# Optimization experiments

Hardware: AMD Instinct MI355X
Metric: run time of the kernel (lower is better)

Reference implementation:

```python
import jax, jax.numpy as jnp
import numpy as np

EMB_DIM = 1024
NUM_HEADS = 16
HEAD_DIM = EMB_DIM // NUM_HEADS  # 64
B, S = 2, 2048


def setup_inputs() -> dict:
    key = jax.random.key(0)
    ks = jax.random.split(key, 9)
    scale = 1.0 / np.sqrt(EMB_DIM)
    return {
        "query": jax.random.normal(ks[0], (B, S, EMB_DIM), dtype=jnp.float32),
        "Wq": jax.random.normal(ks[1], (EMB_DIM, EMB_DIM), dtype=jnp.float32) * scale,
        "bq": jax.random.normal(ks[2], (EMB_DIM,), dtype=jnp.float32) * 0.01,
        "Wk": jax.random.normal(ks[3], (EMB_DIM, EMB_DIM), dtype=jnp.float32) * scale,
        "bk": jax.random.normal(ks[4], (EMB_DIM,), dtype=jnp.float32) * 0.01,
        "Wv": jax.random.normal(ks[5], (EMB_DIM, EMB_DIM), dtype=jnp.float32) * scale,
        "bv": jax.random.normal(ks[6], (EMB_DIM,), dtype=jnp.float32) * 0.01,
        "Wo": jax.random.normal(ks[7], (EMB_DIM, EMB_DIM), dtype=jnp.float32) * scale,
        "bo": jax.random.normal(ks[8], (EMB_DIM,), dtype=jnp.float32) * 0.01,
    }


def reference(query, Wq, bq, Wk, bk, Wv, bv, Wo, bo):
    # Self-attention path (key_value=None, mask=None in the original forward).
    b, s, _ = query.shape
    # torch nn.Linear: y = x @ W.T + b
    def proj(x, W, bias):
        y = jnp.einsum('bse,fe->bsf', x, W) + bias
        # [B,S,E] -> [B,H,S,D]
        return y.reshape(b, s, NUM_HEADS, HEAD_DIM).transpose(0, 2, 1, 3)

    q = proj(query, Wq, bq)
    k = proj(query, Wk, bk)
    v = proj(query, Wv, bv)

    scores = jnp.einsum('bhqd,bhkd->bhqk', q, k) / np.sqrt(HEAD_DIM).astype(np.float32)
    attn = jax.nn.softmax(scores, axis=-1)  # [B,H,S,S]
    out = jnp.einsum('bhqk,bhkd->bhqd', attn, v)
    out = out.transpose(0, 2, 1, 3).reshape(b, s, EMB_DIM)
    return jnp.einsum('bse,fe->bsf', out, Wo) + bo
```

## Files before the change

kernel.cpp:

```cpp
#include <hip/hip_runtime.h>
#include <hip/hip_bf16.h>

using bf16x4 = __attribute__((ext_vector_type(4))) short;
using short8 = __attribute__((ext_vector_type(8))) short;
using f32x4  = __attribute__((ext_vector_type(4))) float;
using u32x2  = __attribute__((ext_vector_type(2))) unsigned;

__device__ __forceinline__ short f2bf(float f) {
  unsigned u = __builtin_bit_cast(unsigned, f);
  u = (u + 0x7fffu + ((u >> 16) & 1u)) >> 16;
  return (short)u;
}
__device__ __forceinline__ unsigned pk2(float a, float b) {
  __hip_bfloat162 h = __float22bfloat162_rn(make_float2(a, b));
  unsigned u; __builtin_memcpy(&u, &h, 4);
  return u;
}
__device__ __forceinline__ void gload16(const short* g, short* l) {
  __builtin_amdgcn_global_load_lds(
      (const __attribute__((address_space(1))) unsigned int*)g,
      (__attribute__((address_space(3))) unsigned int*)l, 16, 0, 0);
}

constexpr int E  = 1024;
constexpr int SL = 2048;
constexpr int NB = 2;
constexpr int NH = 16;
constexpr int M  = NB * SL;

__global__ __launch_bounds__(256) void convert_kernel(
    const float* __restrict__ X,  const float* __restrict__ Wq,
    const float* __restrict__ Wk, const float* __restrict__ Wv,
    const float* __restrict__ Wo, short* __restrict__ out)
{
  const size_t i8 = ((size_t)blockIdx.x * 256 + threadIdx.x) * 8;
  const float* src;
  if (i8 < (size_t)(4u << 20)) {
    src = X + i8;
  } else {
    size_t r = i8 - (size_t)(4u << 20);
    int wi = (int)(r >> 20);
    size_t off = r & ((1u << 20) - 1);
    src = (wi == 0 ? Wq : wi == 1 ? Wk : wi == 2 ? Wv : Wo) + off;
  }
  f32x4 a = *(const f32x4*)src;
  f32x4 b = *(const f32x4*)(src + 4);
  short hb[8];
#pragma unroll
  for (int e = 0; e < 4; ++e) { hb[e] = f2bf(a[e]); hb[4 + e] = f2bf(b[e]); }
  *(short8*)(out + i8) = *(short8*)hb;
}

template <int TM, int TN, bool OUTF32, bool FUSEV>
__global__ __launch_bounds__(256) void gemm_kernel(
    const short* __restrict__ A0, const short* __restrict__ A1, const short* __restrict__ A2,
    const short* __restrict__ W0, const short* __restrict__ W1, const short* __restrict__ W2,
    const float* __restrict__ b0, const float* __restrict__ b1, const float* __restrict__ b2,
    void* __restrict__ Y0, void* __restrict__ Y1, void* __restrict__ Y2,
    float s0, float s1, float s2, int ld0, int ld1, int ld2)
{
  constexpr int BK = 32;
  constexpr int RA = TM / 64;
  constexpr int RB = TN / 64;
  constexpr int WM = TM / 2, WN = TN / 2;
  constexpr int NI = WM / 16, NJ = WN / 16;
  __shared__ alignas(16) short As[2][TM * BK];
  __shared__ alignas(16) short Bs[2][TN * BK];
  const int t = threadIdx.x;
  const int l = t & 63;
  const int w = t >> 6;
  const int c = l & 15;
  const int g = l >> 4;
  const int z = blockIdx.z;
  const short* Ap = (z == 0) ? A0 : (z == 1) ? A1 : A2;
  const short* Wp = (z == 0) ? W0 : (z == 1) ? W1 : W2;
  const float* bp = (z == 0) ? b0 : (z == 1) ? b1 : b2;
  void* Yp        = (z == 0) ? Y0 : (z == 1) ? Y1 : Y2;
  const float sc  = (z == 0) ? s0 : (z == 1) ? s1 : s2;
  const int ldY   = (z == 0) ? ld0 : (z == 1) ? ld1 : ld2;
  const bool vtr  = FUSEV && (z == 2);
  const int m0 = (vtr ? blockIdx.y : blockIdx.x) * TM;
  const int n0 = (vtr ? blockIdx.x : blockIdx.y) * TN;

  const short* gA[RA]; int oA[RA];
  const short* gB[RB]; int oB[RB];
#pragma unroll
  for (int r = 0; r < RA; ++r) {
    const int cc = r * 256 + t;
    gA[r] = Ap + (size_t)(m0 + (cc >> 2)) * E + (cc & 3) * 8;
    oA[r] = (r * 256 + (t & ~63)) * 8;
  }
#pragma unroll
  for (int r = 0; r < RB; ++r) {
    const int cc = r * 256 + t;
    gB[r] = Wp + (size_t)(n0 + (cc >> 2)) * E + (cc & 3) * 8;
    oB[r] = (r * 256 + (t & ~63)) * 8;
  }

#pragma unroll
  for (int r = 0; r < RA; ++r) gload16(gA[r], &As[0][oA[r]]);
#pragma unroll
  for (int r = 0; r < RB; ++r) gload16(gB[r], &Bs[0][oB[r]]);

  const int wm = (w >> 1) * WM;
  const int wn = (w & 1) * WN;
  f32x4 acc[NI][NJ] = {};
  int cur = 0;

  for (int k0 = 0; k0 < E; k0 += BK) {
    __syncthreads();
    if (k0 + BK < E) {
#pragma unroll
      for (int r = 0; r < RA; ++r) gload16(gA[r] + k0 + BK, &As[cur ^ 1][oA[r]]);
#pragma unroll
      for (int r = 0; r < RB; ++r) gload16(gB[r] + k0 + BK, &Bs[cur ^ 1][oB[r]]);
    }
    short8 ah[NI], bfr[NJ];
#pragma unroll
    for (int i = 0; i < NI; ++i)
      ah[i] = *(const short8*)&As[cur][(wm + i * 16 + c) * BK + g * 8];
#pragma unroll
    for (int j = 0; j < NJ; ++j)
      bfr[j] = *(const short8*)&Bs[cur][(wn + j * 16 + c) * BK + g * 8];
#pragma unroll
    for (int i = 0; i < NI; ++i)
#pragma unroll
      for (int j = 0; j < NJ; ++j)
        acc[i][j] = __builtin_amdgcn_mfma_f32_16x16x32_bf16(ah[i], bfr[j], acc[i][j], 0, 0, 0);
    cur ^= 1;
  }

#pragma unroll
  for (int j = 0; j < NJ; ++j) {
    const int col = n0 + wn + j * 16 + c;
    const float bcol = vtr ? 0.f : bp[col];
#pragma unroll
    for (int i = 0; i < NI; ++i) {
      const int rowb = m0 + wm + i * 16 + g * 4;
#pragma unroll
      for (int r = 0; r < 4; ++r) {
        const int row = rowb + r;
        const float bias = vtr ? bp[row] : bcol;
        const float v = (acc[i][j][r] + bias) * sc;
        if (OUTF32) ((float*)Yp)[(size_t)row * ldY + col] = v;
        else        ((short*)Yp)[(size_t)row * ldY + col] = f2bf(v);
      }
    }
  }
}

__global__ __launch_bounds__(256) void flash_kernel(
    const short* __restrict__ Qm, const short* __restrict__ Km,
    const short* __restrict__ VTm, short* __restrict__ Oh)
{
  __shared__ alignas(16) short Ks[2][64][72];
  __shared__ alignas(16) short Vt[2][64][72];
  __shared__ alignas(16) short Pl[4][32][72];
  const int t = threadIdx.x;
  const int l = t & 63;
  const int w = t >> 6;
  const int c = l & 15;
  const int g = l >> 4;
  const int q0 = blockIdx.x * 128;
  const int bh = (int)blockIdx.y;
  const int b = bh >> 4;
  const int hh = bh & 15;
  const size_t baseK = (size_t)b * SL * E + hh * 64;
  const size_t baseV = (size_t)(hh * 64) * M + (size_t)b * SL;

  short8 aq[2][2];
#pragma unroll
  for (int u = 0; u < 2; ++u) {
    const short* qp = Qm + baseK + (size_t)(q0 + w * 32 + u * 16 + c) * E + g * 8;
    aq[u][0] = *(const short8*)qp;
    aq[u][1] = *(const short8*)(qp + 32);
  }

  f32x4 lacc[2] = {{0.f,0.f,0.f,0.f},{0.f,0.f,0.f,0.f}};
  f32x4 acc_o[2][4] = {};

  const int r0 = t >> 3, s0 = t & 7;
  const short* gK0 = Km + baseK + (size_t)r0 * E + s0 * 8;
  const short* gK1 = gK0 + (size_t)32 * E;
  const short* gV0 = VTm + baseV + (size_t)r0 * M + s0 * 8;
  const short* gV1 = gV0 + (size_t)32 * M;

  short8 k0r = *(const short8*)gK0, k1r = *(const short8*)gK1;
  short8 v0r = *(const short8*)gV0, v1r = *(const short8*)gV1;
  *(short8*)&Ks[0][r0][s0 * 8]      = k0r;
  *(short8*)&Ks[0][r0 + 32][s0 * 8] = k1r;
  *(short8*)&Vt[0][r0][s0 * 8]      = v0r;
  *(short8*)&Vt[0][r0 + 32][s0 * 8] = v1r;
  k0r = *(const short8*)(gK0 + (size_t)64 * E);
  k1r = *(const short8*)(gK1 + (size_t)64 * E);
  v0r = *(const short8*)(gV0 + 64);
  v1r = *(const short8*)(gV1 + 64);
  __syncthreads();

  constexpr int NT = SL / 64;
  int cur = 0;
  for (int kt = 0; kt < NT; ++kt) {
    if (kt + 1 < NT) {
      *(short8*)&Ks[cur ^ 1][r0][s0 * 8]      = k0r;
      *(short8*)&Ks[cur ^ 1][r0 + 32][s0 * 8] = k1r;
      *(short8*)&Vt[cur ^ 1][r0][s0 * 8]      = v0r;
      *(short8*)&Vt[cur ^ 1][r0 + 32][s0 * 8] = v1r;
      if (kt + 2 < NT) {
        k0r = *(const short8*)(gK0 + (size_t)(kt + 2) * 64 * E);
        k1r = *(const short8*)(gK1 + (size_t)(kt + 2) * 64 * E);
        v0r = *(const short8*)(gV0 + (kt + 2) * 64);
        v1r = *(const short8*)(gV1 + (kt + 2) * 64);
      }
    }

    short8 kf[4][2];
#pragma unroll
    for (int j = 0; j < 4; ++j)
#pragma unroll
      for (int kc = 0; kc < 2; ++kc)
        kf[j][kc] = *(const short8*)&Ks[cur][j * 16 + c][kc * 32 + g * 8];

    f32x4 st[2][4] = {};
#pragma unroll
    for (int u = 0; u < 2; ++u)
#pragma unroll
      for (int j = 0; j < 4; ++j)
#pragma unroll
        for (int kc = 0; kc < 2; ++kc)
          st[u][j] = __builtin_amdgcn_mfma_f32_16x16x32_bf16(kf[j][kc], aq[u][kc], st[u][j], 0, 0, 0);

#pragma unroll
    for (int u = 0; u < 2; ++u)
#pragma unroll
      for (int j = 0; j < 4; ++j) {
        f32x4 p;
#pragma unroll
        for (int r = 0; r < 4; ++r) p[r] = __builtin_amdgcn_exp2f(st[u][j][r]);
        lacc[u] += p;
        u32x2 pk = {pk2(p[0], p[1]), pk2(p[2], p[3])};
        *(u32x2*)&Pl[w][u * 16 + c][j * 16 + g * 4] = pk;
      }

    short8 ap[2][2];
#pragma unroll
    for (int u = 0; u < 2; ++u) {
      ap[u][0] = *(const short8*)&Pl[w][u * 16 + c][g * 8];
      ap[u][1] = *(const short8*)&Pl[w][u * 16 + c][32 + g * 8];
    }
    short8 vf[4][2];
#pragma unroll
    for (int j = 0; j < 4; ++j)
#pragma unroll
      for (int kc = 0; kc < 2; ++kc)
        vf[j][kc] = *(const short8*)&Vt[cur][j * 16 + c][kc * 32 + g * 8];

#pragma unroll
    for (int u = 0; u < 2; ++u)
#pragma unroll
      for (int j = 0; j < 4; ++j)
#pragma unroll
        for (int kc = 0; kc < 2; ++kc)
          acc_o[u][j] = __builtin_amdgcn_mfma_f32_16x16x32_bf16(vf[j][kc], ap[u][kc], acc_o[u][j], 0, 0, 0);

    __syncthreads();
    cur ^= 1;
  }

#pragma unroll
  for (int u = 0; u < 2; ++u) {
    float s = lacc[u][0] + lacc[u][1] + lacc[u][2] + lacc[u][3];
    s += __shfl_xor(s, 16);
    s += __shfl_xor(s, 32);
    const float inv = 1.0f / s;
    const int token = q0 + w * 32 + u * 16 + c;
    const size_t obase = ((size_t)b * SL + token) * E + hh * 64;
#pragma unroll
    for (int j = 0; j < 4; ++j) {
      u32x2 o2 = {pk2(acc_o[u][j][0] * inv, acc_o[u][j][1] * inv),
                  pk2(acc_o[u][j][2] * inv, acc_o[u][j][3] * inv)};
      *(u32x2*)(Oh + obase + j * 16 + g * 4) = o2;
    }
  }
}

extern "C" void kernel_launch(void* const* d_in, const int* in_sizes, int n_in,
                              void* d_out, int out_size, void* d_ws, size_t ws_size,
                              hipStream_t stream)
{
  const float* X  = (const float*)d_in[0];
  const float* Wq = (const float*)d_in[1];
  const float* bq = (const float*)d_in[2];
  const float* Wk = (const float*)d_in[3];
  const float* bk = (const float*)d_in[4];
  const float* Wv = (const float*)d_in[5];
  const float* bv = (const float*)d_in[6];
  const float* Wo = (const float*)d_in[7];
  const float* bo = (const float*)d_in[8];
  float* out = (float*)d_out;

  const size_t szX = (size_t)M * E;
  const size_t szW = (size_t)E * E;
  short* Xb  = (short*)d_ws;
  short* Wqb = Xb + szX;
  short* Wkb = Wqb + szW;
  short* Wvb = Wkb + szW;
  short* Wob = Wvb + szW;
  short* Qw  = Wob + szW;
  short* Kw  = Qw + szX;
  short* VTw = Kw + szX;

  convert_kernel<<<4096, 256, 0, stream>>>(X, Wq, Wk, Wv, Wo, Xb);

  const float kLog2eOver8 = 0.18033688011112042f;
  dim3 g1(M / 128, E / 128, 3);
  gemm_kernel<128, 128, false, true><<<g1, 256, 0, stream>>>(
      Xb, Xb, Wvb,
      Wqb, Wkb, Xb,
      bq, bk, bv,
      (void*)Qw, (void*)Kw, (void*)VTw,
      kLog2eOver8, 1.0f, 1.0f, E, E, M);

  dim3 g2(SL / 128, NB * NH);
  flash_kernel<<<g2, 256, 0, stream>>>(Qw, Kw, VTw, Qw );

  dim3 g3(M / 128, E / 64, 1);
  gemm_kernel<128, 64, true, false><<<g3, 256, 0, stream>>>(
      Qw, Qw, Qw,
      Wob, Wob, Wob,
      bo, bo, bo,
      (void*)out, (void*)out, (void*)out,
      1.0f, 1.0f, 1.0f, E, E, E);
}
```

Before: 213.9 us.

## Split flash attention along the key dimension with a separate combine pass

The flash kernel now splits the 2048 keys into two halves along a new grid z dimension. This doubles the block count from 512 to 1024 to improve occupancy on the many CUs. Each half writes unnormalized bf16 partial outputs and row sums, and a new combine kernel adds the halves and normalizes them. This works without a running max because the softmax has no max subtraction. The K/V staging drops double buffering in favour of a single buffer with two barriers per tile, and adds a launch bound asking for higher occupancy. The cost is an extra kernel launch, extra memory traffic for the partials, and one more bf16 rounding of the partial outputs.

```diff
diff --git a/kernel.cpp b/kernel.cpp
--- a/kernel.cpp
+++ b/kernel.cpp
@@ -10,6 +10,10 @@
   unsigned u = __builtin_bit_cast(unsigned, f);
   u = (u + 0x7fffu + ((u >> 16) & 1u)) >> 16;
   return (short)u;
+}
+__device__ __forceinline__ float bf2f(short s) {
+  unsigned u = ((unsigned)(unsigned short)s) << 16;
+  return __builtin_bit_cast(float, u);
 }
 __device__ __forceinline__ unsigned pk2(float a, float b) {
   __hip_bfloat162 h = __float22bfloat162_rn(make_float2(a, b));
@@ -27,28 +31,33 @@
 constexpr int NB = 2;
 constexpr int NH = 16;
 constexpr int M  = NB * SL;
+constexpr size_t MM = 1u << 20;
 
 __global__ __launch_bounds__(256) void convert_kernel(
     const float* __restrict__ X,  const float* __restrict__ Wq,
     const float* __restrict__ Wk, const float* __restrict__ Wv,
-    const float* __restrict__ Wo, short* __restrict__ out)
+    const float* __restrict__ Wo, short* __restrict__ out,
+    short* __restrict__ outWo)
 {
   const size_t i8 = ((size_t)blockIdx.x * 256 + threadIdx.x) * 8;
-  const float* src;
-  if (i8 < (size_t)(4u << 20)) {
-    src = X + i8;
+  const float* src; short* dst;
+  if (i8 < 4 * MM) {
+    src = X + i8; dst = out + i8;
   } else {
-    size_t r = i8 - (size_t)(4u << 20);
+    size_t r = i8 - 4 * MM;
     int wi = (int)(r >> 20);
-    size_t off = r & ((1u << 20) - 1);
-    src = (wi == 0 ? Wq : wi == 1 ? Wk : wi == 2 ? Wv : Wo) + off;
+    size_t off = r & (MM - 1);
+    if      (wi == 0) { src = Wq + off; dst = out + 4 * MM + off; }
+    else if (wi == 1) { src = Wk + off; dst = out + 5 * MM + off; }
+    else if (wi == 2) { src = Wv + off; dst = out + 6 * MM + off; }
+    else              { src = Wo + off; dst = outWo + off; }
   }
   f32x4 a = *(const f32x4*)src;
   f32x4 b = *(const f32x4*)(src + 4);
   short hb[8];
 #pragma unroll
   for (int e = 0; e < 4; ++e) { hb[e] = f2bf(a[e]); hb[4 + e] = f2bf(b[e]); }
-  *(short8*)(out + i8) = *(short8*)hb;
+  *(short8*)dst = *(short8*)hb;
 }
 
 template <int TM, int TN, bool OUTF32, bool FUSEV>
@@ -149,12 +158,14 @@
   }
 }
 
-__global__ __launch_bounds__(256) void flash_kernel(
+__global__ __launch_bounds__(256, 4) void flash_kernel(
     const short* __restrict__ Qm, const short* __restrict__ Km,
-    const short* __restrict__ VTm, short* __restrict__ Oh)
-{
-  __shared__ alignas(16) short Ks[2][64][72];
-  __shared__ alignas(16) short Vt[2][64][72];
+    const short* __restrict__ VTm, short* __restrict__ O1,
+    short* __restrict__ O2a, short* __restrict__ O2b,
+    float* __restrict__ lpart)
+{
+  __shared__ alignas(16) short Ks[64][72];
+  __shared__ alignas(16) short Vt[64][72];
   __shared__ alignas(16) short Pl[4][32][72];
   const int t = threadIdx.x;
   const int l = t & 63;
@@ -165,6 +176,7 @@
   const int bh = (int)blockIdx.y;
   const int b = bh >> 4;
   const int hh = bh & 15;
+  const int ks = (int)blockIdx.z;
   const size_t baseK = (size_t)b * SL * E + hh * 64;
   const size_t baseV = (size_t)(hh * 64) * M + (size_t)b * SL;
 
@@ -179,38 +191,27 @@
   f32x4 lacc[2] = {{0.f,0.f,0.f,0.f},{0.f,0.f,0.f,0.f}};
   f32x4 acc_o[2][4] = {};
 
-  const int r0 = t >> 3, s0 = t & 7;
-  const short* gK0 = Km + baseK + (size_t)r0 * E + s0 * 8;
+  const int r0 = t >> 3, sg = t & 7;
+  const short* gK0 = Km + baseK + (size_t)(ks * 1024 + r0) * E + sg * 8;
   const short* gK1 = gK0 + (size_t)32 * E;
-  const short* gV0 = VTm + baseV + (size_t)r0 * M + s0 * 8;
+  const short* gV0 = VTm + baseV + (size_t)r0 * M + ks * 1024 + sg * 8;
   const short* gV1 = gV0 + (size_t)32 * M;
 
   short8 k0r = *(const short8*)gK0, k1r = *(const short8*)gK1;
   short8 v0r = *(const short8*)gV0, v1r = *(const short8*)gV1;
-  *(short8*)&Ks[0][r0][s0 * 8]      = k0r;
-  *(short8*)&Ks[0][r0 + 32][s0 * 8] = k1r;
-  *(short8*)&Vt[0][r0][s0 * 8]      = v0r;
-  *(short8*)&Vt[0][r0 + 32][s0 * 8] = v1r;
-  k0r = *(const short8*)(gK0 + (size_t)64 * E);
-  k1r = *(const short8*)(gK1 + (size_t)64 * E);
-  v0r = *(const short8*)(gV0 + 64);
-  v1r = *(const short8*)(gV1 + 64);
-  __syncthreads();
-
-  constexpr int NT = SL / 64;
-  int cur = 0;
-  for (int kt = 0; kt < NT; ++kt) {
-    if (kt + 1 < NT) {
-      *(short8*)&Ks[cur ^ 1][r0][s0 * 8]      = k0r;
-      *(short8*)&Ks[cur ^ 1][r0 + 32][s0 * 8] = k1r;
-      *(short8*)&Vt[cur ^ 1][r0][s0 * 8]      = v0r;
-      *(short8*)&Vt[cur ^ 1][r0 + 32][s0 * 8] = v1r;
-      if (kt + 2 < NT) {
-        k0r = *(const short8*)(gK0 + (size_t)(kt + 2) * 64 * E);
-        k1r = *(const short8*)(gK1 + (size_t)(kt + 2) * 64 * E);
-        v0r = *(const short8*)(gV0 + (kt + 2) * 64);
-        v1r = *(const short8*)(gV1 + (kt + 2) * 64);
-      }
+
+  for (int kt = 0; kt < 16; ++kt) {
+    __syncthreads();
+    *(short8*)&Ks[r0][sg * 8]      = k0r;
+    *(short8*)&Ks[r0 + 32][sg * 8] = k1r;
+    *(short8*)&Vt[r0][sg * 8]      = v0r;
+    *(short8*)&Vt[r0 + 32][sg * 8] = v1r;
+    __syncthreads();
+    if (kt + 1 < 16) {
+      k0r = *(const short8*)(gK0 + (size_t)(kt + 1) * 64 * E);
+      k1r = *(const short8*)(gK1 + (size_t)(kt + 1) * 64 * E);
+      v0r = *(const short8*)(gV0 + (kt + 1) * 64);
+      v1r = *(const short8*)(gV1 + (kt + 1) * 64);
     }
 
     short8 kf[4][2];
@@ -218,7 +219,7 @@
     for (int j = 0; j < 4; ++j)
 #pragma unroll
       for (int kc = 0; kc < 2; ++kc)
-        kf[j][kc] = *(const short8*)&Ks[cur][j * 16 + c][kc * 32 + g * 8];
+        kf[j][kc] = *(const short8*)&Ks[j * 16 + c][kc * 32 + g * 8];
 
     f32x4 st[2][4] = {};
 #pragma unroll
@@ -252,7 +253,7 @@
     for (int j = 0; j < 4; ++j)
 #pragma unroll
       for (int kc = 0; kc < 2; ++kc)
-        vf[j][kc] = *(const short8*)&Vt[cur][j * 16 + c][kc * 32 + g * 8];
+        vf[j][kc] = *(const short8*)&Vt[j * 16 + c][kc * 32 + g * 8];
 
 #pragma unroll
     for (int u = 0; u < 2; ++u)
@@ -261,9 +262,6 @@
 #pragma unroll
         for (int kc = 0; kc < 2; ++kc)
           acc_o[u][j] = __builtin_amdgcn_mfma_f32_16x16x32_bf16(vf[j][kc], ap[u][kc], acc_o[u][j], 0, 0, 0);
-
-    __syncthreads();
-    cur ^= 1;
   }
 
 #pragma unroll
@@ -271,16 +269,38 @@
     float s = lacc[u][0] + lacc[u][1] + lacc[u][2] + lacc[u][3];
     s += __shfl_xor(s, 16);
     s += __shfl_xor(s, 32);
-    const float inv = 1.0f / s;
-    const int token = q0 + w * 32 + u * 16 + c;
-    const size_t obase = ((size_t)b * SL + token) * E + hh * 64;
+    const int fr = b * SL + q0 + w * 32 + u * 16 + c;
+    if (g == 0) lpart[(size_t)ks * 65536 + (size_t)fr * 16 + hh] = s;
+    short* OB; size_t off;
+    if (ks == 0)          { OB = O1;  off = (size_t)fr * E + hh * 64; }
+    else if (fr < 3072)   { OB = O2a; off = (size_t)fr * E + hh * 64; }
+    else                  { OB = O2b; off = (size_t)(fr - 3072) * E + hh * 64; }
 #pragma unroll
     for (int j = 0; j < 4; ++j) {
-      u32x2 o2 = {pk2(acc_o[u][j][0] * inv, acc_o[u][j][1] * inv),
-                  pk2(acc_o[u][j][2] * inv, acc_o[u][j][3] * inv)};
-      *(u32x2*)(Oh + obase + j * 16 + g * 4) = o2;
-    }
-  }
+      u32x2 o2 = {pk2(acc_o[u][j][0], acc_o[u][j][1]),
+                  pk2(acc_o[u][j][2], acc_o[u][j][3])};
+      *(u32x2*)(OB + off + j * 16 + g * 4) = o2;
+    }
+  }
+}
+
+__global__ __launch_bounds__(256) void combine_kernel(
+    const short* __restrict__ O1, const short* __restrict__ O2a,
+    const short* __restrict__ O2b, const float* __restrict__ lpart,
+    short* __restrict__ Oh)
+{
+  const size_t i8 = ((size_t)blockIdx.x * 256 + threadIdx.x) * 8;
+  const size_t fr = i8 >> 10;
+  const int h = (int)((i8 >> 6) & 15);
+  const float linv = 1.0f / (lpart[fr * 16 + h] + lpart[65536 + fr * 16 + h]);
+  short8 a = *(const short8*)(O1 + i8);
+  short8 bb = (fr < 3072) ? *(const short8*)(O2a + i8)
+                          : *(const short8*)(O2b + (i8 - (size_t)3072 * 1024));
+  short hb[8];
+#pragma unroll
+  for (int e = 0; e < 8; ++e)
+    hb[e] = f2bf((bf2f(a[e]) + bf2f(bb[e])) * linv);
+  *(short8*)(Oh + i8) = *(short8*)hb;
 }
 
 extern "C" void kernel_launch(void* const* d_in, const int* in_sizes, int n_in,
@@ -298,18 +318,20 @@
   const float* bo = (const float*)d_in[8];
   float* out = (float*)d_out;
 
-  const size_t szX = (size_t)M * E;
-  const size_t szW = (size_t)E * E;
-  short* Xb  = (short*)d_ws;
-  short* Wqb = Xb + szX;
-  short* Wkb = Wqb + szW;
-  short* Wvb = Wkb + szW;
-  short* Wob = Wvb + szW;
-  short* Qw  = Wob + szW;
-  short* Kw  = Qw + szX;
-  short* VTw = Kw + szX;
-
-  convert_kernel<<<4096, 256, 0, stream>>>(X, Wq, Wk, Wv, Wo, Xb);
+  short* Xb   = (short*)d_ws;
+  short* Wqb  = Xb + 4 * MM;
+  short* Wkb  = Wqb + MM;
+  short* Wvb  = Wkb + MM;
+  short* Qw   = Wvb + MM;
+  short* Kw   = Qw + 4 * MM;
+  short* VTw  = Kw + 4 * MM;
+  short* Wob  = VTw + 4 * MM;
+  float* lpart = (float*)(Wob + MM);
+  short* O2b  = (short*)(lpart + 131072);
+  short* O1   = Xb;
+  short* O2a  = Wqb;
+
+  convert_kernel<<<4096, 256, 0, stream>>>(X, Wq, Wk, Wv, Wo, Xb, Wob);
 
   const float kLog2eOver8 = 0.18033688011112042f;
   dim3 g1(M / 128, E / 128, 3);
@@ -320,8 +342,10 @@
       (void*)Qw, (void*)Kw, (void*)VTw,
       kLog2eOver8, 1.0f, 1.0f, E, E, M);
 
-  dim3 g2(SL / 128, NB * NH);
-  flash_kernel<<<g2, 256, 0, stream>>>(Qw, Kw, VTw, Qw );
+  dim3 g2(SL / 128, NB * NH, 2);
+  flash_kernel<<<g2, 256, 0, stream>>>(Qw, Kw, VTw, O1, O2a, O2b, lpart);
+
+  combine_kernel<<<(M * E / 8) / 256, 256, 0, stream>>>(O1, O2a, O2b, lpart, Qw);
 
   dim3 g3(M / 128, E / 64, 1);
   gemm_kernel<128, 64, true, false><<<g3, 256, 0, stream>>>(
```

Result: no change. 211.6 us (-1.1%).
